# Performance work log

Measured on AMD Instinct MI355X. Metric: run time of the kernel, lower is better.

## Reference

```python
import jax, jax.numpy as jnp
import numpy as np

C = 128      # block channels
K = 7        # involution kernel size
GC = 16      # group_ch
G = (C // 2) // GC  # involution groups = 4


def conv1x1(x, w, b):
    # x: (B,Cin,H,W), w: (Cout,Cin)
    return jnp.einsum('bchw,oc->bohw', x, w) + b[None, :, None, None]


def conv2d(x, w, b, pad):
    y = jax.lax.conv_general_dilated(
        x, w, window_strides=(1, 1), padding=((pad, pad), (pad, pad)),
        dimension_numbers=('NCHW', 'OIHW', 'NCHW'))
    return y + b[None, :, None, None]


def prelu(x, a):
    return jnp.where(x >= 0, x, a * x)


def patches7(x):
    # x: (B,C,H,W) -> (B,C,K*K,H,W), same padding (torch Unfold, pad=3)
    B, Cc, H, W = x.shape
    p = K // 2
    xp = jnp.pad(x, ((0, 0), (0, 0), (p, p), (p, p)))
    return jnp.stack([xp[:, :, i:i + H, j:j + W]
                      for i in range(K) for j in range(K)], axis=2)


def setup_inputs() -> dict:
    key = jax.random.key(0)
    ks = jax.random.split(key, 9)
    f32 = jnp.float32
    def w(k, shape, s=0.02):
        return jax.random.normal(k, shape, f32) * s
    d = {}
    d['x'] = jax.random.normal(ks[0], (2, C, 128, 128), f32)
    # conv1: C -> C//2, 1x1
    d['w1'] = w(ks[1], (C // 2, C)); d['b1'] = jnp.zeros((C // 2,), f32)
    d['a1'] = jnp.float32(0.25)  # PReLU (single param)
    # involution reduce: C//2 -> C//4, 1x1 (+ReLU)
    d['wr'] = w(ks[2], (C // 4, C // 2)); d['br'] = jnp.zeros((C // 4,), f32)
    # involution span: C//4 -> G*K*K, 1x1
    d['ws'] = w(ks[3], (G * K * K, C // 4)); d['bs'] = jnp.zeros((G * K * K,), f32)
    d['a2'] = jnp.float32(0.25)
    # conv2: C//2 -> C, 1x1
    d['w2'] = w(ks[4], (C, C // 2)); d['b2'] = jnp.zeros((C,), f32)
    # attn conv: 2 -> 1, 7x7 pad 3
    d['wa'] = w(ks[5], (1, 2, 7, 7)); d['ba'] = jnp.zeros((1,), f32)
    # psec: 3x3 (C//4->C//4) + PReLU + 1x1 (C//4->C)
    d['wp1'] = w(ks[6], (C // 4, C // 4, 3, 3)); d['bp1'] = jnp.zeros((C // 4,), f32)
    d['ap'] = jnp.float32(0.25)
    d['wp2'] = w(ks[7], (C, C // 4)); d['bp2'] = jnp.zeros((C,), f32)
    return d


def reference(x, w1, b1, a1, wr, br, ws, bs, a2, w2, b2, wa, ba, wp1, bp1, ap, wp2, bp2):
    B, _, H, W = x.shape
    x1 = prelu(conv1x1(x, w1, b1), a1)                       # (B, C/2, H, W)
    # involution: per-pixel dynamic kernels
    f = jax.nn.relu(conv1x1(x1, wr, br))                     # (B, C/4, H, W)
    kw = conv1x1(f, ws, bs).reshape(B, G, 1, K * K, H, W)    # dynamic kernels
    pat = patches7(x1).reshape(B, G, GC, K * K, H, W)        # unfolded patches
    x2 = (kw * pat).sum(axis=3).reshape(B, C // 2, H, W)     # multiply-reduce
    x3 = conv1x1(prelu(x2, a2), w2, b2)                      # (B, C, H, W)
    # attention gate on f (ZPool -> 7x7 conv -> sigmoid)
    zp = jnp.concatenate([f.max(axis=1, keepdims=True),
                          f.mean(axis=1, keepdims=True)], axis=1)
    attn = jax.nn.sigmoid(conv2d(zp, wa, ba, 3))             # (B, 1, H, W)
    x4 = x3 * attn
    ps = conv1x1(prelu(conv2d(f, wp1, bp1, 1), ap), wp2, bp2)
    return x4 + ps
```

## Files before the change

kernel.cpp:

```cpp
#include <hip/hip_runtime.h>

#define HW_  16384
#define NPX  32768
#define NPG  8192

__device__ __forceinline__ float prelu_(float x, float a) { return x >= 0.f ? x : a * x; }

__global__ __launch_bounds__(256, 4) void k_conv1(const float* __restrict__ x,
        const float* __restrict__ w1, const float* __restrict__ b1,
        const float* __restrict__ a1p, float* __restrict__ x1) {
    int tid = blockIdx.x * 256 + threadIdx.x;
    int pg = tid & (NPG - 1);
    int q = tid >> 13;
    int b = pg >> 12;
    int hw = (pg & 4095) << 2;
    int o0 = q * 4;
    const float a1 = a1p[0];
    float4 acc[4];
    #pragma unroll
    for (int u = 0; u < 4; ++u) { float bv = b1[o0 + u]; acc[u] = make_float4(bv, bv, bv, bv); }
    const float4* xp = (const float4*)(x + (b << 21) + hw);
    #pragma unroll 1
    for (int cb = 0; cb < 8; ++cb) {
        float4 xv[16];
        #pragma unroll
        for (int j = 0; j < 16; ++j) xv[j] = xp[(cb * 16 + j) << 12];
        #pragma unroll
        for (int j = 0; j < 16; ++j) {
            int c = cb * 16 + j;
            #pragma unroll
            for (int u = 0; u < 4; ++u) {
                float wv = w1[(o0 + u) * 128 + c];
                acc[u].x = fmaf(wv, xv[j].x, acc[u].x);
                acc[u].y = fmaf(wv, xv[j].y, acc[u].y);
                acc[u].z = fmaf(wv, xv[j].z, acc[u].z);
                acc[u].w = fmaf(wv, xv[j].w, acc[u].w);
            }
        }
    }
    float4* op = (float4*)(x1 + (b << 20) + hw);
    #pragma unroll
    for (int u = 0; u < 4; ++u) {
        float4 r;
        r.x = prelu_(acc[u].x, a1); r.y = prelu_(acc[u].y, a1);
        r.z = prelu_(acc[u].z, a1); r.w = prelu_(acc[u].w, a1);
        op[(o0 + u) << 12] = r;
    }
}

__global__ __launch_bounds__(256, 4) void k_reduce(const float* __restrict__ x1,
        const float* __restrict__ wr, const float* __restrict__ br,
        float* __restrict__ f) {
    int tid = blockIdx.x * 256 + threadIdx.x;
    int p2 = tid & 16383;
    int q = tid >> 14;
    int b = p2 >> 13;
    int hw = (p2 & 8191) << 1;
    int o0 = q * 4;
    float2 acc[4];
    #pragma unroll
    for (int u = 0; u < 4; ++u) { float bv = br[o0 + u]; acc[u] = make_float2(bv, bv); }
    const float2* xp = (const float2*)(x1 + (b << 20) + hw);
    #pragma unroll 1
    for (int cb = 0; cb < 4; ++cb) {
        float2 xv[16];
        #pragma unroll
        for (int j = 0; j < 16; ++j) xv[j] = xp[(cb * 16 + j) << 13];
        #pragma unroll
        for (int j = 0; j < 16; ++j) {
            int c = cb * 16 + j;
            #pragma unroll
            for (int u = 0; u < 4; ++u) {
                float wv = wr[(o0 + u) * 64 + c];
                acc[u].x = fmaf(wv, xv[j].x, acc[u].x);
                acc[u].y = fmaf(wv, xv[j].y, acc[u].y);
            }
        }
    }
    float2* op = (float2*)(f + (b << 19) + hw);
    #pragma unroll
    for (int u = 0; u < 4; ++u) {
        float2 r;
        r.x = fmaxf(acc[u].x, 0.f); r.y = fmaxf(acc[u].y, 0.f);
        op[(o0 + u) << 13] = r;
    }
}

__global__ __launch_bounds__(256) void k_invol(const float* __restrict__ x1,
        const float* __restrict__ f, const float* __restrict__ ws_,
        const float* __restrict__ bs, float* __restrict__ x2,
        float* __restrict__ zp) {
    __shared__ float tile[16 * 22 * 24];
    int g = blockIdx.x >> 7;
    int t = blockIdx.x & 127;
    int b = t >> 6;
    int th = (t >> 3) & 7, tw = t & 7;
    int h0 = th * 16, w0 = tw * 16;
    const float* x1g = x1 + ((b * 64 + g * 16) << 14);
    #pragma unroll 1
    for (int rem = threadIdx.x; rem < 484; rem += 256) {
        int r = rem / 22, cl = rem - r * 22;
        int hh = h0 + r - 3, ww = w0 + cl - 3;
        bool ok = (hh >= 0 && hh < 128 && ww >= 0 && ww < 128);
        const float* src = x1g + (hh << 7) + ww;
        float v[16];
        #pragma unroll
        for (int c = 0; c < 16; ++c) v[c] = ok ? src[c << 14] : 0.f;
        float* dst = tile + r * 24 + cl;
        #pragma unroll
        for (int c = 0; c < 16; ++c) dst[c * 528] = v[c];
    }
    int lh = threadIdx.x >> 4, lw = threadIdx.x & 15;
    int hw = ((h0 + lh) << 7) + w0 + lw;
    float fv[32];
    const float* fp = f + (b << 19) + hw;
    #pragma unroll
    for (int c = 0; c < 32; ++c) fv[c] = fp[c << 14];
    if (g == 0) {
        float mx = fv[0], sm = fv[0];
        #pragma unroll
        for (int c = 1; c < 32; ++c) { mx = fmaxf(mx, fv[c]); sm += fv[c]; }
        zp[((b * 2 + 0) << 14) + hw] = mx;
        zp[((b * 2 + 1) << 14) + hw] = sm * (1.f / 32.f);
    }
    __syncthreads();
    float acc[16];
    #pragma unroll
    for (int u = 0; u < 16; ++u) acc[u] = 0.f;
    const float* tap0 = tile + lh * 24 + lw;
    const float* wk = ws_ + g * 49 * 32;
    const float* bsg = bs + g * 49;
    #pragma unroll 1
    for (int di = 0; di < 7; ++di) {
        #pragma unroll 1
        for (int dj = 0; dj < 7; ++dj) {
            int kk = di * 7 + dj;
            float kwv = bsg[kk];
            const float* wkk = wk + kk * 32;
            #pragma unroll
            for (int c = 0; c < 32; ++c) kwv = fmaf(wkk[c], fv[c], kwv);
            const float* tp = tap0 + di * 24 + dj;
            #pragma unroll
            for (int u = 0; u < 16; ++u)
                acc[u] = fmaf(kwv, tp[u * 528], acc[u]);
        }
    }
    float* op = x2 + ((b * 64 + g * 16) << 14) + hw;
    #pragma unroll
    for (int u = 0; u < 16; ++u) op[u << 14] = acc[u];
}

__global__ __launch_bounds__(256) void k_attn(const float* __restrict__ zp,
        const float* __restrict__ wa, const float* __restrict__ ba,
        float* __restrict__ attn) {
    __shared__ float zs[2][22 * 23];
    int t = blockIdx.x;
    int b = t >> 6;
    int tile = t & 63;
    int th = tile >> 3, tw = tile & 7;
    int h0 = th * 16, w0 = tw * 16;
    const float* zb = zp + (b << 15);
    #pragma unroll 1
    for (int rem = threadIdx.x; rem < 484; rem += 256) {
        int r = rem / 22, cl = rem - r * 22;
        int hh = h0 + r - 3, ww = w0 + cl - 3;
        bool ok = (hh >= 0 && hh < 128 && ww >= 0 && ww < 128);
        const float* src = zb + (hh << 7) + ww;
        float v0 = ok ? src[0] : 0.f;
        float v1 = ok ? src[HW_] : 0.f;
        zs[0][r * 23 + cl] = v0;
        zs[1][r * 23 + cl] = v1;
    }
    __syncthreads();
    int lh = threadIdx.x >> 4, lw = threadIdx.x & 15;
    float acc = ba[0];
    #pragma unroll
    for (int c = 0; c < 2; ++c) {
        const float* zc = &zs[c][lh * 23 + lw];
        #pragma unroll
        for (int i = 0; i < 7; ++i)
            #pragma unroll
            for (int j = 0; j < 7; ++j)
                acc = fmaf(wa[c * 49 + i * 7 + j], zc[i * 23 + j], acc);
    }
    attn[(b << 14) + ((h0 + lh) << 7) + w0 + lw] = 1.f / (1.f + expf(-acc));
}

__global__ __launch_bounds__(256) void k_psec1(const float* __restrict__ f,
        const float* __restrict__ wp1, const float* __restrict__ bp1,
        const float* __restrict__ app, float* __restrict__ p1) {
    __shared__ float fs[32 * 18 * 19];
    __shared__ float wT[288 * 16];
    int half = blockIdx.x >> 7;
    int t = blockIdx.x & 127;
    int b = t >> 6;
    int tile = t & 63;
    int th = tile >> 3, tw = tile & 7;
    int h0 = th * 16, w0 = tw * 16;
    int o0 = half * 16;

    const float4* wsrc4 = (const float4*)(wp1 + o0 * 288);
    #pragma unroll 1
    for (int e4 = threadIdx.x; e4 < 1152; e4 += 256) {
        float4 v = wsrc4[e4];
        int o = e4 / 72, r4 = (e4 - o * 72) * 4;
        wT[(r4 + 0) * 16 + o] = v.x;
        wT[(r4 + 1) * 16 + o] = v.y;
        wT[(r4 + 2) * 16 + o] = v.z;
        wT[(r4 + 3) * 16 + o] = v.w;
    }
    const float* fb = f + (b << 19);
    #pragma unroll 1
    for (int rem = threadIdx.x; rem < 324; rem += 256) {
        int r = rem / 18, cl = rem - r * 18;
        int hh = h0 + r - 1, ww = w0 + cl - 1;
        bool ok = (hh >= 0 && hh < 128 && ww >= 0 && ww < 128);
        const float* src = fb + (hh << 7) + ww;
        float* dst = fs + r * 19 + cl;
        #pragma unroll 1
        for (int cb = 0; cb < 4; ++cb) {
            float v[8];
            #pragma unroll
            for (int c = 0; c < 8; ++c) v[c] = ok ? src[(cb * 8 + c) << 14] : 0.f;
            #pragma unroll
            for (int c = 0; c < 8; ++c) dst[(cb * 8 + c) * 342] = v[c];
        }
    }
    __syncthreads();

    int pxq = threadIdx.x & 63;
    int rowq = pxq >> 2, colq = pxq & 3;
    int oh = threadIdx.x >> 6;
    const float ap = app[0];
    float acc[4][4];
    #pragma unroll
    for (int o = 0; o < 4; ++o) {
        float bv = bp1[o0 + oh * 4 + o];
        #pragma unroll
        for (int px = 0; px < 4; ++px) acc[o][px] = bv;
    }
    const float* fsb = fs + rowq * 19 + colq * 4;
    for (int ci = 0; ci < 32; ++ci) {
        float tap[3][6];
        const float* base = fsb + ci * 342;
        #pragma unroll
        for (int r = 0; r < 3; ++r)
            #pragma unroll
            for (int j = 0; j < 6; ++j)
                tap[r][j] = base[r * 19 + j];
        #pragma unroll
        for (int ki = 0; ki < 3; ++ki)
            #pragma unroll
            for (int kj = 0; kj < 3; ++kj) {
                const float* wv = &wT[((ci * 9 + ki * 3 + kj) << 4) + oh * 4];
                float w0v = wv[0], w1v = wv[1], w2v = wv[2], w3v = wv[3];
                #pragma unroll
                for (int px = 0; px < 4; ++px) {
                    float tv = tap[ki][px + kj];
                    acc[0][px] = fmaf(w0v, tv, acc[0][px]);
                    acc[1][px] = fmaf(w1v, tv, acc[1][px]);
                    acc[2][px] = fmaf(w2v, tv, acc[2][px]);
                    acc[3][px] = fmaf(w3v, tv, acc[3][px]);
                }
            }
    }
    int hw = ((h0 + rowq) << 7) + w0 + colq * 4;
    #pragma unroll
    for (int o = 0; o < 4; ++o) {
        float4 r;
        r.x = prelu_(acc[o][0], ap); r.y = prelu_(acc[o][1], ap);
        r.z = prelu_(acc[o][2], ap); r.w = prelu_(acc[o][3], ap);
        *(float4*)(p1 + ((b * 32 + o0 + oh * 4 + o) << 14) + hw) = r;
    }
}

__global__ __launch_bounds__(256, 4) void k_final(const float* __restrict__ x2,
        const float* __restrict__ p1, const float* __restrict__ attn,
        const float* __restrict__ a2p, const float* __restrict__ w2,
        const float* __restrict__ b2, const float* __restrict__ wp2,
        const float* __restrict__ bp2, float* __restrict__ out) {
    int tid = blockIdx.x * 256 + threadIdx.x;
    int pg = tid & (NPG - 1);
    int q = tid >> 13;
    int b = pg >> 12;
    int hw = (pg & 4095) << 2;
    int o0 = q * 4;
    const float a2 = a2p[0];
    float4 acc[4];
    #pragma unroll
    for (int u = 0; u < 4; ++u) { float bv = b2[o0 + u]; acc[u] = make_float4(bv, bv, bv, bv); }
    const float4* xp = (const float4*)(x2 + (b << 20) + hw);
    #pragma unroll 1
    for (int cb = 0; cb < 4; ++cb) {
        float4 xv[16];
        #pragma unroll
        for (int j = 0; j < 16; ++j) xv[j] = xp[(cb * 16 + j) << 12];
        #pragma unroll
        for (int j = 0; j < 16; ++j) {
            float4 v = xv[j];
            v.x = prelu_(v.x, a2); v.y = prelu_(v.y, a2);
            v.z = prelu_(v.z, a2); v.w = prelu_(v.w, a2);
            int c = cb * 16 + j;
            #pragma unroll
            for (int u = 0; u < 4; ++u) {
                float wv = w2[(o0 + u) * 64 + c];
                acc[u].x = fmaf(wv, v.x, acc[u].x);
                acc[u].y = fmaf(wv, v.y, acc[u].y);
                acc[u].z = fmaf(wv, v.z, acc[u].z);
                acc[u].w = fmaf(wv, v.w, acc[u].w);
            }
        }
    }
    float4 at = ((const float4*)attn)[pg];
    #pragma unroll
    for (int u = 0; u < 4; ++u) {
        float bv = bp2[o0 + u];
        acc[u].x = acc[u].x * at.x + bv;
        acc[u].y = acc[u].y * at.y + bv;
        acc[u].z = acc[u].z * at.z + bv;
        acc[u].w = acc[u].w * at.w + bv;
    }
    const float4* pp = (const float4*)(p1 + (b << 19) + hw);
    #pragma unroll 1
    for (int cb = 0; cb < 2; ++cb) {
        float4 pv[16];
        #pragma unroll
        for (int j = 0; j < 16; ++j) pv[j] = pp[(cb * 16 + j) << 12];
        #pragma unroll
        for (int j = 0; j < 16; ++j) {
            int c = cb * 16 + j;
            #pragma unroll
            for (int u = 0; u < 4; ++u) {
                float wv = wp2[(o0 + u) * 32 + c];
                acc[u].x = fmaf(wv, pv[j].x, acc[u].x);
                acc[u].y = fmaf(wv, pv[j].y, acc[u].y);
                acc[u].z = fmaf(wv, pv[j].z, acc[u].z);
                acc[u].w = fmaf(wv, pv[j].w, acc[u].w);
            }
        }
    }
    float4* op = (float4*)(out + ((b * 128 + o0) << 14) + hw);
    #pragma unroll
    for (int u = 0; u < 4; ++u) op[u << 12] = acc[u];
}

extern "C" void kernel_launch(void* const* d_in, const int* in_sizes, int n_in,
                              void* d_out, int out_size, void* d_ws, size_t ws_size,
                              hipStream_t stream) {
    const float* x   = (const float*)d_in[0];
    const float* w1  = (const float*)d_in[1];
    const float* b1  = (const float*)d_in[2];
    const float* a1  = (const float*)d_in[3];
    const float* wr  = (const float*)d_in[4];
    const float* br  = (const float*)d_in[5];
    const float* ws_ = (const float*)d_in[6];
    const float* bs  = (const float*)d_in[7];
    const float* a2  = (const float*)d_in[8];
    const float* w2  = (const float*)d_in[9];
    const float* b2  = (const float*)d_in[10];
    const float* wa  = (const float*)d_in[11];
    const float* ba  = (const float*)d_in[12];
    const float* wp1 = (const float*)d_in[13];
    const float* bp1 = (const float*)d_in[14];
    const float* ap  = (const float*)d_in[15];
    const float* wp2 = (const float*)d_in[16];
    const float* bp2 = (const float*)d_in[17];
    float* out = (float*)d_out;

    float* w = (float*)d_ws;
    float* ws_x1   = w;
    float* ws_f    = ws_x1 + 2 * 64 * HW_;
    float* ws_x2   = ws_f  + 2 * 32 * HW_;
    float* ws_zp   = ws_x2 + 2 * 64 * HW_;
    float* ws_attn = ws_zp + 2 * 2 * HW_;
    float* ws_p1   = ws_attn + NPX;

    hipLaunchKernelGGL(k_conv1, dim3(16 * NPG / 256), dim3(256), 0, stream,
                       x, w1, b1, a1, ws_x1);
    hipLaunchKernelGGL(k_reduce, dim3(8 * 16384 / 256), dim3(256), 0, stream,
                       ws_x1, wr, br, ws_f);
    hipLaunchKernelGGL(k_invol, dim3(512), dim3(256), 0, stream,
                       ws_x1, ws_f, ws_, bs, ws_x2, ws_zp);
    hipLaunchKernelGGL(k_attn, dim3(128), dim3(256), 0, stream,
                       ws_zp, wa, ba, ws_attn);
    hipLaunchKernelGGL(k_psec1, dim3(256), dim3(256), 0, stream,
                       ws_f, wp1, bp1, ap, ws_p1);
    hipLaunchKernelGGL(k_final, dim3(32 * NPG / 256), dim3(256), 0, stream,
                       ws_x2, ws_p1, ws_attn, a2, w2, b2, wp2, bp2, out);
}
```

Before: 209.6 us.

## Tile conv1 and final 1x1 convs through shared memory; shrink psec1 tiles

Rewrites k_conv1 and k_final so each block stages a 128-pixel tile of all input channels in LDS, along with transposed weights. Each thread then computes 4 outputs by 4 pixels from LDS instead of every thread rereading the global activations for its own 4 output channels. The aim is to cut redundant global reads of x and x2 (previously reread 16 or 32 times across output groups) and the scalar weight loads. k_psec1 uses 8-row tiles with 2 outputs per thread to double the block count, at the cost of more halo reloads. The large LDS footprint and launch_bounds(…,2) lower occupancy.

After: 194.5 us. -7.2%, faster.

```diff
diff --git a/kernel.cpp b/kernel.cpp
--- a/kernel.cpp
+++ b/kernel.cpp
@@ -2,49 +2,67 @@
 
 #define HW_  16384
 #define NPX  32768
-#define NPG  8192
 
 __device__ __forceinline__ float prelu_(float x, float a) { return x >= 0.f ? x : a * x; }
 
-__global__ __launch_bounds__(256, 4) void k_conv1(const float* __restrict__ x,
+__global__ __launch_bounds__(256, 2) void k_conv1(const float* __restrict__ x,
         const float* __restrict__ w1, const float* __restrict__ b1,
         const float* __restrict__ a1p, float* __restrict__ x1) {
-    int tid = blockIdx.x * 256 + threadIdx.x;
-    int pg = tid & (NPG - 1);
-    int q = tid >> 13;
-    int b = pg >> 12;
-    int hw = (pg & 4095) << 2;
-    int o0 = q * 4;
+    __shared__ float xs[64 * 128];
+    __shared__ float wT[128 * 36];
+    int split = blockIdx.x >> 8;
+    int tile = blockIdx.x & 255;
+    int b = tile >> 7;
+    int hw0 = (tile & 127) << 7;
+    int o0 = split * 32;
+
+    for (int e = threadIdx.x; e < 4096; e += 256) {
+        int o = e >> 7, c = e & 127;
+        wT[c * 36 + o] = w1[(o0 + o) * 128 + c];
+    }
+    int pxq = threadIdx.x & 31, outq = threadIdx.x >> 5;
     const float a1 = a1p[0];
     float4 acc[4];
     #pragma unroll
-    for (int u = 0; u < 4; ++u) { float bv = b1[o0 + u]; acc[u] = make_float4(bv, bv, bv, bv); }
-    const float4* xp = (const float4*)(x + (b << 21) + hw);
-    #pragma unroll 1
-    for (int cb = 0; cb < 8; ++cb) {
-        float4 xv[16];
-        #pragma unroll
-        for (int j = 0; j < 16; ++j) xv[j] = xp[(cb * 16 + j) << 12];
-        #pragma unroll
-        for (int j = 0; j < 16; ++j) {
-            int c = cb * 16 + j;
-            #pragma unroll
-            for (int u = 0; u < 4; ++u) {
-                float wv = w1[(o0 + u) * 128 + c];
-                acc[u].x = fmaf(wv, xv[j].x, acc[u].x);
-                acc[u].y = fmaf(wv, xv[j].y, acc[u].y);
-                acc[u].z = fmaf(wv, xv[j].z, acc[u].z);
-                acc[u].w = fmaf(wv, xv[j].w, acc[u].w);
-            }
-        }
-    }
-    float4* op = (float4*)(x1 + (b << 20) + hw);
+    for (int u = 0; u < 4; ++u) { float bv = b1[o0 + outq * 4 + u]; acc[u] = make_float4(bv, bv, bv, bv); }
+    const float4* xb = (const float4*)(x + (b << 21) + hw0);
+    #pragma unroll 1
+    for (int half = 0; half < 2; ++half) {
+        float4 xv[8];
+        #pragma unroll
+        for (int i = 0; i < 8; ++i) {
+            int e = threadIdx.x + i * 256;
+            int ch = e >> 5, pq = e & 31;
+            xv[i] = xb[((half * 64 + ch) << 12) + pq];
+        }
+        #pragma unroll
+        for (int i = 0; i < 8; ++i) {
+            int e = threadIdx.x + i * 256;
+            int ch = e >> 5, pq = e & 31;
+            *(float4*)&xs[ch * 128 + pq * 4] = xv[i];
+        }
+        __syncthreads();
+        #pragma unroll 8
+        for (int c2 = 0; c2 < 64; ++c2) {
+            float4 tap = *(const float4*)&xs[c2 * 128 + pxq * 4];
+            float4 wv  = *(const float4*)&wT[(half * 64 + c2) * 36 + outq * 4];
+            acc[0].x = fmaf(wv.x, tap.x, acc[0].x); acc[0].y = fmaf(wv.x, tap.y, acc[0].y);
+            acc[0].z = fmaf(wv.x, tap.z, acc[0].z); acc[0].w = fmaf(wv.x, tap.w, acc[0].w);
+            acc[1].x = fmaf(wv.y, tap.x, acc[1].x); acc[1].y = fmaf(wv.y, tap.y, acc[1].y);
+            acc[1].z = fmaf(wv.y, tap.z, acc[1].z); acc[1].w = fmaf(wv.y, tap.w, acc[1].w);
+            acc[2].x = fmaf(wv.z, tap.x, acc[2].x); acc[2].y = fmaf(wv.z, tap.y, acc[2].y);
+            acc[2].z = fmaf(wv.z, tap.z, acc[2].z); acc[2].w = fmaf(wv.z, tap.w, acc[2].w);
+            acc[3].x = fmaf(wv.w, tap.x, acc[3].x); acc[3].y = fmaf(wv.w, tap.y, acc[3].y);
+            acc[3].z = fmaf(wv.w, tap.z, acc[3].z); acc[3].w = fmaf(wv.w, tap.w, acc[3].w);
+        }
+        __syncthreads();
+    }
     #pragma unroll
     for (int u = 0; u < 4; ++u) {
         float4 r;
         r.x = prelu_(acc[u].x, a1); r.y = prelu_(acc[u].y, a1);
         r.z = prelu_(acc[u].z, a1); r.w = prelu_(acc[u].w, a1);
-        op[(o0 + u) << 12] = r;
+        *(float4*)(x1 + ((b * 64 + o0 + outq * 4 + u) << 14) + hw0 + pxq * 4) = r;
     }
 }
 
@@ -189,14 +207,14 @@
 __global__ __launch_bounds__(256) void k_psec1(const float* __restrict__ f,
         const float* __restrict__ wp1, const float* __restrict__ bp1,
         const float* __restrict__ app, float* __restrict__ p1) {
-    __shared__ float fs[32 * 18 * 19];
+    __shared__ float fs[32 * 190];
     __shared__ float wT[288 * 16];
-    int half = blockIdx.x >> 7;
-    int t = blockIdx.x & 127;
-    int b = t >> 6;
-    int tile = t & 63;
+    int half = blockIdx.x >> 8;
+    int t = blockIdx.x & 255;
+    int b = t >> 7;
+    int tile = t & 127;
     int th = tile >> 3, tw = tile & 7;
-    int h0 = th * 16, w0 = tw * 16;
+    int h0 = th * 8, w0 = tw * 16;
     int o0 = half * 16;
 
     const float4* wsrc4 = (const float4*)(wp1 + o0 * 288);
@@ -211,7 +229,7 @@
     }
     const float* fb = f + (b << 19);
     #pragma unroll 1
-    for (int rem = threadIdx.x; rem < 324; rem += 256) {
+    for (int rem = threadIdx.x; rem < 180; rem += 256) {
         int r = rem / 18, cl = rem - r * 18;
         int hh = h0 + r - 1, ww = w0 + cl - 1;
         bool ok = (hh >= 0 && hh < 128 && ww >= 0 && ww < 128);
@@ -223,26 +241,26 @@
             #pragma unroll
             for (int c = 0; c < 8; ++c) v[c] = ok ? src[(cb * 8 + c) << 14] : 0.f;
             #pragma unroll
-            for (int c = 0; c < 8; ++c) dst[(cb * 8 + c) * 342] = v[c];
+            for (int c = 0; c < 8; ++c) dst[(cb * 8 + c) * 190] = v[c];
         }
     }
     __syncthreads();
 
-    int pxq = threadIdx.x & 63;
+    int pxq = threadIdx.x & 31;
     int rowq = pxq >> 2, colq = pxq & 3;
-    int oh = threadIdx.x >> 6;
+    int oh = threadIdx.x >> 5;
     const float ap = app[0];
-    float acc[4][4];
-    #pragma unroll
-    for (int o = 0; o < 4; ++o) {
-        float bv = bp1[o0 + oh * 4 + o];
+    float acc[2][4];
+    #pragma unroll
+    for (int o = 0; o < 2; ++o) {
+        float bv = bp1[o0 + oh * 2 + o];
         #pragma unroll
         for (int px = 0; px < 4; ++px) acc[o][px] = bv;
     }
     const float* fsb = fs + rowq * 19 + colq * 4;
     for (int ci = 0; ci < 32; ++ci) {
         float tap[3][6];
-        const float* base = fsb + ci * 342;
+        const float* base = fsb + ci * 190;
         #pragma unroll
         for (int r = 0; r < 3; ++r)
             #pragma unroll
@@ -252,96 +270,127 @@
         for (int ki = 0; ki < 3; ++ki)
             #pragma unroll
             for (int kj = 0; kj < 3; ++kj) {
-                const float* wv = &wT[((ci * 9 + ki * 3 + kj) << 4) + oh * 4];
-                float w0v = wv[0], w1v = wv[1], w2v = wv[2], w3v = wv[3];
+                float2 wv = *(const float2*)&wT[((ci * 9 + ki * 3 + kj) << 4) + oh * 2];
                 #pragma unroll
                 for (int px = 0; px < 4; ++px) {
                     float tv = tap[ki][px + kj];
-                    acc[0][px] = fmaf(w0v, tv, acc[0][px]);
-                    acc[1][px] = fmaf(w1v, tv, acc[1][px]);
-                    acc[2][px] = fmaf(w2v, tv, acc[2][px]);
-                    acc[3][px] = fmaf(w3v, tv, acc[3][px]);
+                    acc[0][px] = fmaf(wv.x, tv, acc[0][px]);
+                    acc[1][px] = fmaf(wv.y, tv, acc[1][px]);
                 }
             }
     }
     int hw = ((h0 + rowq) << 7) + w0 + colq * 4;
     #pragma unroll
-    for (int o = 0; o < 4; ++o) {
+    for (int o = 0; o < 2; ++o) {
         float4 r;
         r.x = prelu_(acc[o][0], ap); r.y = prelu_(acc[o][1], ap);
         r.z = prelu_(acc[o][2], ap); r.w = prelu_(acc[o][3], ap);
-        *(float4*)(p1 + ((b * 32 + o0 + oh * 4 + o) << 14) + hw) = r;
-    }
-}
-
-__global__ __launch_bounds__(256, 4) void k_final(const float* __restrict__ x2,
+        *(float4*)(p1 + ((b * 32 + o0 + oh * 2 + o) << 14) + hw) = r;
+    }
+}
+
+__global__ __launch_bounds__(256, 2) void k_final(const float* __restrict__ x2,
         const float* __restrict__ p1, const float* __restrict__ attn,
         const float* __restrict__ a2p, const float* __restrict__ w2,
         const float* __restrict__ b2, const float* __restrict__ wp2,
         const float* __restrict__ bp2, float* __restrict__ out) {
-    int tid = blockIdx.x * 256 + threadIdx.x;
-    int pg = tid & (NPG - 1);
-    int q = tid >> 13;
-    int b = pg >> 12;
-    int hw = (pg & 4095) << 2;
-    int o0 = q * 4;
+    __shared__ float xs2[64 * 128];
+    __shared__ float ps[32 * 128];
+    __shared__ float wT2[64 * 36];
+    __shared__ float wTp[32 * 36];
+    __shared__ float as_[128];
+    int split = blockIdx.x >> 8;
+    int tile = blockIdx.x & 255;
+    int b = tile >> 7;
+    int hw0 = (tile & 127) << 7;
+    int o0 = split * 32;
     const float a2 = a2p[0];
-    float4 acc[4];
-    #pragma unroll
-    for (int u = 0; u < 4; ++u) { float bv = b2[o0 + u]; acc[u] = make_float4(bv, bv, bv, bv); }
-    const float4* xp = (const float4*)(x2 + (b << 20) + hw);
-    #pragma unroll 1
-    for (int cb = 0; cb < 4; ++cb) {
-        float4 xv[16];
-        #pragma unroll
-        for (int j = 0; j < 16; ++j) xv[j] = xp[(cb * 16 + j) << 12];
-        #pragma unroll
-        for (int j = 0; j < 16; ++j) {
-            float4 v = xv[j];
+
+    for (int e = threadIdx.x; e < 2048; e += 256) {
+        int o = e >> 6, c = e & 63;
+        wT2[c * 36 + o] = w2[(o0 + o) * 64 + c];
+    }
+    for (int e = threadIdx.x; e < 1024; e += 256) {
+        int o = e >> 5, c = e & 31;
+        wTp[c * 36 + o] = wp2[(o0 + o) * 32 + c];
+    }
+    {
+        const float4* xb = (const float4*)(x2 + (b << 20) + hw0);
+        float4 xv[8];
+        #pragma unroll
+        for (int i = 0; i < 8; ++i) {
+            int e = threadIdx.x + i * 256;
+            xv[i] = xb[((e >> 5) << 12) + (e & 31)];
+        }
+        #pragma unroll
+        for (int i = 0; i < 8; ++i) {
+            int e = threadIdx.x + i * 256;
+            float4 v = xv[i];
             v.x = prelu_(v.x, a2); v.y = prelu_(v.y, a2);
             v.z = prelu_(v.z, a2); v.w = prelu_(v.w, a2);
-            int c = cb * 16 + j;
-            #pragma unroll
-            for (int u = 0; u < 4; ++u) {
-                float wv = w2[(o0 + u) * 64 + c];
-                acc[u].x = fmaf(wv, v.x, acc[u].x);
-                acc[u].y = fmaf(wv, v.y, acc[u].y);
-                acc[u].z = fmaf(wv, v.z, acc[u].z);
-                acc[u].w = fmaf(wv, v.w, acc[u].w);
-            }
-        }
-    }
-    float4 at = ((const float4*)attn)[pg];
+            *(float4*)&xs2[(e >> 5) * 128 + (e & 31) * 4] = v;
+        }
+        const float4* pb = (const float4*)(p1 + (b << 19) + hw0);
+        float4 pv[4];
+        #pragma unroll
+        for (int i = 0; i < 4; ++i) {
+            int e = threadIdx.x + i * 256;
+            pv[i] = pb[((e >> 5) << 12) + (e & 31)];
+        }
+        #pragma unroll
+        for (int i = 0; i < 4; ++i) {
+            int e = threadIdx.x + i * 256;
+            *(float4*)&ps[(e >> 5) * 128 + (e & 31) * 4] = pv[i];
+        }
+        if (threadIdx.x < 32)
+            ((float4*)as_)[threadIdx.x] = ((const float4*)(attn + (b << 14) + hw0))[threadIdx.x];
+    }
+    int pxq = threadIdx.x & 31, outq = threadIdx.x >> 5;
+    float b2v[4], bpv[4];
+    #pragma unroll
+    for (int u = 0; u < 4; ++u) { b2v[u] = b2[o0 + outq * 4 + u]; bpv[u] = bp2[o0 + outq * 4 + u]; }
+    __syncthreads();
+
+    float4 acc[4];
+    #pragma unroll
+    for (int u = 0; u < 4; ++u) acc[u] = make_float4(0.f, 0.f, 0.f, 0.f);
+    #pragma unroll 8
+    for (int c = 0; c < 64; ++c) {
+        float4 tap = *(const float4*)&xs2[c * 128 + pxq * 4];
+        float4 wv  = *(const float4*)&wT2[c * 36 + outq * 4];
+        acc[0].x = fmaf(wv.x, tap.x, acc[0].x); acc[0].y = fmaf(wv.x, tap.y, acc[0].y);
+        acc[0].z = fmaf(wv.x, tap.z, acc[0].z); acc[0].w = fmaf(wv.x, tap.w, acc[0].w);
+        acc[1].x = fmaf(wv.y, tap.x, acc[1].x); acc[1].y = fmaf(wv.y, tap.y, acc[1].y);
+        acc[1].z = fmaf(wv.y, tap.z, acc[1].z); acc[1].w = fmaf(wv.y, tap.w, acc[1].w);
+        acc[2].x = fmaf(wv.z, tap.x, acc[2].x); acc[2].y = fmaf(wv.z, tap.y, acc[2].y);
+        acc[2].z = fmaf(wv.z, tap.z, acc[2].z); acc[2].w = fmaf(wv.z, tap.w, acc[2].w);
+        acc[3].x = fmaf(wv.w, tap.x, acc[3].x); acc[3].y = fmaf(wv.w, tap.y, acc[3].y);
+        acc[3].z = fmaf(wv.w, tap.z, acc[3].z); acc[3].w = fmaf(wv.w, tap.w, acc[3].w);
+    }
+    float4 at = *(const float4*)&as_[pxq * 4];
     #pragma unroll
     for (int u = 0; u < 4; ++u) {
-        float bv = bp2[o0 + u];
-        acc[u].x = acc[u].x * at.x + bv;
-        acc[u].y = acc[u].y * at.y + bv;
-        acc[u].z = acc[u].z * at.z + bv;
-        acc[u].w = acc[u].w * at.w + bv;
-    }
-    const float4* pp = (const float4*)(p1 + (b << 19) + hw);
-    #pragma unroll 1
-    for (int cb = 0; cb < 2; ++cb) {
-        float4 pv[16];
-        #pragma unroll
-        for (int j = 0; j < 16; ++j) pv[j] = pp[(cb * 16 + j) << 12];
-        #pragma unroll
-        for (int j = 0; j < 16; ++j) {
-            int c = cb * 16 + j;
-            #pragma unroll
-            for (int u = 0; u < 4; ++u) {
-                float wv = wp2[(o0 + u) * 32 + c];
-                acc[u].x = fmaf(wv, pv[j].x, acc[u].x);
-                acc[u].y = fmaf(wv, pv[j].y, acc[u].y);
-                acc[u].z = fmaf(wv, pv[j].z, acc[u].z);
-                acc[u].w = fmaf(wv, pv[j].w, acc[u].w);
-            }
-        }
-    }
-    float4* op = (float4*)(out + ((b * 128 + o0) << 14) + hw);
-    #pragma unroll
-    for (int u = 0; u < 4; ++u) op[u << 12] = acc[u];
+        acc[u].x = (acc[u].x + b2v[u]) * at.x + bpv[u];
+        acc[u].y = (acc[u].y + b2v[u]) * at.y + bpv[u];
+        acc[u].z = (acc[u].z + b2v[u]) * at.z + bpv[u];
+        acc[u].w = (acc[u].w + b2v[u]) * at.w + bpv[u];
+    }
+    #pragma unroll 8
+    for (int c = 0; c < 32; ++c) {
+        float4 tap = *(const float4*)&ps[c * 128 + pxq * 4];
+        float4 wv  = *(const float4*)&wTp[c * 36 + outq * 4];
+        acc[0].x = fmaf(wv.x, tap.x, acc[0].x); acc[0].y = fmaf(wv.x, tap.y, acc[0].y);
+        acc[0].z = fmaf(wv.x, tap.z, acc[0].z); acc[0].w = fmaf(wv.x, tap.w, acc[0].w);
+        acc[1].x = fmaf(wv.y, tap.x, acc[1].x); acc[1].y = fmaf(wv.y, tap.y, acc[1].y);
+        acc[1].z = fmaf(wv.y, tap.z, acc[1].z); acc[1].w = fmaf(wv.y, tap.w, acc[1].w);
+        acc[2].x = fmaf(wv.z, tap.x, acc[2].x); acc[2].y = fmaf(wv.z, tap.y, acc[2].y);
+        acc[2].z = fmaf(wv.z, tap.z, acc[2].z); acc[2].w = fmaf(wv.z, tap.w, acc[2].w);
+        acc[3].x = fmaf(wv.w, tap.x, acc[3].x); acc[3].y = fmaf(wv.w, tap.y, acc[3].y);
+        acc[3].z = fmaf(wv.w, tap.z, acc[3].z); acc[3].w = fmaf(wv.w, tap.w, acc[3].w);
+    }
+    #pragma unroll
+    for (int u = 0; u < 4; ++u)
+        *(float4*)(out + ((b * 128 + o0 + outq * 4 + u) << 14) + hw0 + pxq * 4) = acc[u];
 }
 
 extern "C" void kernel_launch(void* const* d_in, const int* in_sizes, int n_in,
@@ -375,7 +424,7 @@
     float* ws_attn = ws_zp + 2 * 2 * HW_;
     float* ws_p1   = ws_attn + NPX;
 
-    hipLaunchKernelGGL(k_conv1, dim3(16 * NPG / 256), dim3(256), 0, stream,
+    hipLaunchKernelGGL(k_conv1, dim3(512), dim3(256), 0, stream,
                        x, w1, b1, a1, ws_x1);
     hipLaunchKernelGGL(k_reduce, dim3(8 * 16384 / 256), dim3(256), 0, stream,
                        ws_x1, wr, br, ws_f);
@@ -383,8 +432,8 @@
                        ws_x1, ws_f, ws_, bs, ws_x2, ws_zp);
     hipLaunchKernelGGL(k_attn, dim3(128), dim3(256), 0, stream,
                        ws_zp, wa, ba, ws_attn);
-    hipLaunchKernelGGL(k_psec1, dim3(256), dim3(256), 0, stream,
+    hipLaunchKernelGGL(k_psec1, dim3(512), dim3(256), 0, stream,
                        ws_f, wp1, bp1, ap, ws_p1);
-    hipLaunchKernelGGL(k_final, dim3(32 * NPG / 256), dim3(256), 0, stream,
+    hipLaunchKernelGGL(k_final, dim3(1024), dim3(256), 0, stream,
                        ws_x2, ws_p1, ws_attn, a2, w2, b2, wp2, bp2, out);
 }
```
